# Kernel optimization log

Measured on AMD Instinct MI355X. Metric: run time of the kernel, lower is better.

The kernel has to match this reference:

```python
import jax, jax.numpy as jnp
import numpy as np

B, S, D_IN = 128, 196, 512
H, DK, RATIO = 8, 32, 4
DV = RATIO * DK                      # 128
QKV_DIM = H * (2 * DK + DV)          # 1536
PROJ_IN = H * DV                     # 1024
EPS = 1e-3                           # keras BatchNormalization default epsilon
SCALE = DK ** (-0.5)


def hard_swish(x):
    return x * jnp.clip(x + 3.0, 0.0, 6.0) * (1.0 / 6.0)


def setup_inputs() -> dict:
    key = jax.random.key(0)
    ks = jax.random.split(key, 12)
    inp = {
        "x": jax.random.normal(ks[0], (B, S, D_IN), dtype=jnp.float32),
        "W_qkv": jax.random.normal(ks[1], (D_IN, QKV_DIM), dtype=jnp.float32) * (D_IN ** -0.5),
        "b_qkv": jnp.zeros((QKV_DIM,), dtype=jnp.float32),
        "gamma1": jnp.ones((QKV_DIM,), dtype=jnp.float32),
        "beta1": jnp.zeros((QKV_DIM,), dtype=jnp.float32),
        "mean1": jax.random.normal(ks[2], (QKV_DIM,), dtype=jnp.float32) * 0.1,
        "var1": jax.random.uniform(ks[3], (QKV_DIM,), minval=0.5, maxval=1.5, dtype=jnp.float32),
        "W_proj": jax.random.normal(ks[4], (PROJ_IN, D_IN), dtype=jnp.float32) * (PROJ_IN ** -0.5),
        "b_proj": jnp.zeros((D_IN,), dtype=jnp.float32),
        "gamma2": jnp.ones((D_IN,), dtype=jnp.float32),
        "beta2": jnp.zeros((D_IN,), dtype=jnp.float32),
        "mean2": jax.random.normal(ks[5], (D_IN,), dtype=jnp.float32) * 0.1,
        "var2": jax.random.uniform(ks[6], (D_IN,), minval=0.5, maxval=1.5, dtype=jnp.float32),
    }
    return inp


def _bn(x, gamma, beta, mean, var):
    # inference-mode BatchNorm over the last (channel) axis
    return (x - mean) * jax.lax.rsqrt(var + EPS) * gamma + beta


def reference(x, W_qkv, b_qkv, gamma1, beta1, mean1, var1,
              W_proj, b_proj, gamma2, beta2, mean2, var2):
    # QKV projection + BN
    qkv = _bn(x @ W_qkv + b_qkv, gamma1, beta1, mean1, var1)      # [B,S,1536]
    qkv = qkv.reshape(B, S, H, 2 * DK + DV)
    q, k, v = jnp.split(qkv, [DK, 2 * DK], axis=3)                # [B,S,H,*]
    q = jnp.transpose(q, (0, 2, 1, 3))                            # [B,H,S,DK]
    k = jnp.transpose(k, (0, 2, 1, 3))
    v = jnp.transpose(v, (0, 2, 1, 3))                            # [B,H,S,DV]
    attn = jax.nn.softmax(jnp.einsum("bhqd,bhkd->bhqk", q, k) * SCALE, axis=-1)
    av = jnp.einsum("bhqk,bhkd->bhqd", attn, v)                   # [B,H,S,DV]
    # faithful to original: transpose to [B,H,DV,S] then reshape to [B,S,H*DV]
    hidden = jnp.transpose(av, (0, 1, 3, 2)).reshape(B, S, PROJ_IN)
    hidden = hard_swish(hidden)
    out = _bn(hidden @ W_proj + b_proj, gamma2, beta2, mean2, var2)  # [B,S,512]
    return out
```

## Files before the change

### kernel.cpp

```cpp
#include <hip/hip_runtime.h>
#include <math.h>

namespace {

constexpr int Bb   = 128;
constexpr int Ss   = 196;
constexpr int DIN  = 512;
constexpr int Hh   = 8;
constexpr int DKc  = 32;
constexpr int DVc  = 128;
constexpr int QKVD = 1536;
constexpr int PIN  = 1024;
constexpr int Mrows = Bb * Ss;
constexpr float EPSc   = 1e-3f;
constexpr float SCALEc = 0.17677669529663687f;

typedef __bf16 bf16x8 __attribute__((ext_vector_type(8)));
typedef __bf16 bf16x4 __attribute__((ext_vector_type(4)));
typedef float  f32x4  __attribute__((ext_vector_type(4)));

constexpr int VT_STRIDE = 232;
constexpr size_t VT_QELEMS = 8192;
constexpr size_t VT_BH = 4 * VT_QELEMS;

__device__ __forceinline__ void gl_lds16(const void* g, void* l) {
    __builtin_amdgcn_global_load_lds(
        (const __attribute__((address_space(1))) void*)g,
        (__attribute__((address_space(3))) void*)l, 16, 0, 0);
}

__global__ __launch_bounds__(256)
void cvt_f32_bf16(const float* __restrict__ in, __bf16* __restrict__ out, int n4)
{
    int i = blockIdx.x * 256 + threadIdx.x;
    if (i < n4) {
        float4 v = ((const float4*)in)[i];
        bf16x4 o = { (__bf16)v.x, (__bf16)v.y, (__bf16)v.z, (__bf16)v.w };
        ((bf16x4*)out)[i] = o;
    }
}

__global__ __launch_bounds__(256)
void transpose_cvt(const float* __restrict__ W, __bf16* __restrict__ WT, int K, int N)
{
    __shared__ float tile[32][33];
    const int n0 = blockIdx.x * 32, k0 = blockIdx.y * 32;
    const int tx = threadIdx.x & 31, ty = threadIdx.x >> 5;
#pragma unroll
    for (int i = ty; i < 32; i += 8)
        tile[i][tx] = W[(size_t)(k0 + i) * N + n0 + tx];
    __syncthreads();
#pragma unroll
    for (int i = ty; i < 32; i += 8)
        WT[(size_t)(n0 + i) * K + k0 + tx] = (__bf16)tile[tx][i];
}

__global__ __launch_bounds__(256)
void gemm1_bn_scatter(const __bf16* __restrict__ A, const __bf16* __restrict__ BT,
                      const float* __restrict__ bias, const float* __restrict__ gamma,
                      const float* __restrict__ beta, const float* __restrict__ mean,
                      const float* __restrict__ var,
                      __bf16* __restrict__ qkvO, __bf16* __restrict__ VTp)
{
    constexpr int N = QKVD, K = DIN;
    constexpr int BM = 128, BN = 128, BK = 32;
    __shared__ __bf16 As[BM * BK];
    __shared__ __bf16 Bs[BN * BK];

    const int t    = threadIdx.x;
    const int wave = t >> 6;
    const int lane = t & 63;
    const int lr   = lane & 15;
    const int q    = lane >> 4;

    constexpr int ntiles = N / BN;
    const int m0 = (int)(blockIdx.x / ntiles) * BM;
    const int n0 = (int)(blockIdx.x % ntiles) * BN;
    const int wm = (wave & 1) * 64;
    const int wn = (wave >> 1) * 64;

    const __bf16* aG0 = A  + (size_t)(m0 + (t >> 2)) * K + (t & 3) * 8;
    const __bf16* aG1 = aG0 + (size_t)64 * K;
    const __bf16* bG0 = BT + (size_t)(n0 + (t >> 2)) * K + (t & 3) * 8;
    const __bf16* bG1 = bG0 + (size_t)64 * K;
    char* lA = (char*)As + wave * 1024;
    char* lB = (char*)Bs + wave * 1024;

    f32x4 acc[4][4] = {};

    for (int k0 = 0; k0 < K; k0 += BK) {
        gl_lds16(aG0 + k0, lA);
        gl_lds16(aG1 + k0, lA + 4096);
        gl_lds16(bG0 + k0, lB);
        gl_lds16(bG1 + k0, lB + 4096);
        __syncthreads();
        bf16x8 aF[4], bF[4];
#pragma unroll
        for (int i = 0; i < 4; ++i)
            aF[i] = *(const bf16x8*)(As + (wm + i * 16 + lr) * 32 + q * 8);
#pragma unroll
        for (int j = 0; j < 4; ++j)
            bF[j] = *(const bf16x8*)(Bs + (wn + j * 16 + lr) * 32 + q * 8);
#pragma unroll
        for (int i = 0; i < 4; ++i)
#pragma unroll
            for (int j = 0; j < 4; ++j)
                acc[i][j] = __builtin_amdgcn_mfma_f32_16x16x32_bf16(
                    aF[i], bF[j], acc[i][j], 0, 0, 0);
        __syncthreads();
    }

    int bidx[4], sidx[4];
#pragma unroll
    for (int i = 0; i < 4; ++i) {
        int mrow = m0 + wm + i * 16 + q * 4;
        bidx[i] = mrow / 196;
        sidx[i] = mrow - bidx[i] * 196;
    }
#pragma unroll
    for (int j = 0; j < 4; ++j) {
        const int n  = n0 + wn + j * 16 + lr;
        const int h  = n / 192;
        const int ch = n - h * 192;
        const float s  = gamma[n] * rsqrtf(var[n] + EPSc);
        const float tv = fmaf(bias[n] - mean[n], s, beta[n]);
        if (ch < 64) {
#pragma unroll
            for (int i = 0; i < 4; ++i) {
                const int mrow = m0 + wm + i * 16 + q * 4;
#pragma unroll
                for (int r = 0; r < 4; ++r)
                    qkvO[(size_t)(mrow + r) * N + n] = (__bf16)fmaf(acc[i][j][r], s, tv);
            }
        } else {
            const int d = ch - 64;
#pragma unroll
            for (int i = 0; i < 4; ++i) {
                const size_t base = (size_t)(bidx[i] * 8 + h) * VT_BH
                                  + (size_t)(d >> 5) * VT_QELEMS
                                  + (size_t)(d & 31) * VT_STRIDE + sidx[i];
                bf16x4 pk = { (__bf16)fmaf(acc[i][j][0], s, tv),
                              (__bf16)fmaf(acc[i][j][1], s, tv),
                              (__bf16)fmaf(acc[i][j][2], s, tv),
                              (__bf16)fmaf(acc[i][j][3], s, tv) };
                *(bf16x4*)(VTp + base) = pk;
            }
        }
    }
}

template<int N, int K>
__global__ __launch_bounds__(256)
void gemm_bn_mfma(const __bf16* __restrict__ A, const __bf16* __restrict__ BT,
                  const float* __restrict__ bias, const float* __restrict__ gamma,
                  const float* __restrict__ beta, const float* __restrict__ mean,
                  const float* __restrict__ var, float* __restrict__ C)
{
    constexpr int BM = 128, BN = 128, BK = 32;
    __shared__ __bf16 As[BM * BK];
    __shared__ __bf16 Bs[BN * BK];
    const int t    = threadIdx.x;
    const int wave = t >> 6;
    const int lane = t & 63;
    const int lr   = lane & 15;
    const int q    = lane >> 4;
    constexpr int ntiles = N / BN;
    const int m0 = (int)(blockIdx.x / ntiles) * BM;
    const int n0 = (int)(blockIdx.x % ntiles) * BN;
    const int wm = (wave & 1) * 64;
    const int wn = (wave >> 1) * 64;
    const __bf16* aG0 = A  + (size_t)(m0 + (t >> 2)) * K + (t & 3) * 8;
    const __bf16* aG1 = aG0 + (size_t)64 * K;
    const __bf16* bG0 = BT + (size_t)(n0 + (t >> 2)) * K + (t & 3) * 8;
    const __bf16* bG1 = bG0 + (size_t)64 * K;
    char* lA = (char*)As + wave * 1024;
    char* lB = (char*)Bs + wave * 1024;
    f32x4 acc[4][4] = {};
    for (int k0 = 0; k0 < K; k0 += BK) {
        gl_lds16(aG0 + k0, lA);
        gl_lds16(aG1 + k0, lA + 4096);
        gl_lds16(bG0 + k0, lB);
        gl_lds16(bG1 + k0, lB + 4096);
        __syncthreads();
        bf16x8 aF[4], bF[4];
#pragma unroll
        for (int i = 0; i < 4; ++i)
            aF[i] = *(const bf16x8*)(As + (wm + i * 16 + lr) * 32 + q * 8);
#pragma unroll
        for (int j = 0; j < 4; ++j)
            bF[j] = *(const bf16x8*)(Bs + (wn + j * 16 + lr) * 32 + q * 8);
#pragma unroll
        for (int i = 0; i < 4; ++i)
#pragma unroll
            for (int j = 0; j < 4; ++j)
                acc[i][j] = __builtin_amdgcn_mfma_f32_16x16x32_bf16(
                    aF[i], bF[j], acc[i][j], 0, 0, 0);
        __syncthreads();
    }
#pragma unroll
    for (int j = 0; j < 4; ++j) {
        const int n = n0 + wn + j * 16 + lr;
        const float s  = gamma[n] * rsqrtf(var[n] + EPSc);
        const float tv = fmaf(bias[n] - mean[n], s, beta[n]);
#pragma unroll
        for (int i = 0; i < 4; ++i) {
            const int mrow = m0 + wm + i * 16 + q * 4;
#pragma unroll
            for (int r = 0; r < 4; ++r)
                C[(size_t)(mrow + r) * N + n] = fmaf(acc[i][j][r], s, tv);
        }
    }
}

__global__ __launch_bounds__(1024)
void attn_mfma(const __bf16* __restrict__ qkv, const __bf16* __restrict__ VTp,
               __bf16* __restrict__ hidden)
{
    __shared__ __align__(16) char smem[145920];
    __bf16* Kb = (__bf16*)smem;

    const int t = threadIdx.x;
    const int wave = t >> 6, lane = t & 63;
    const int lr = lane & 15, q = lane >> 4;
    const int bh = blockIdx.x;
    const int b = bh >> 3, h = bh & 7;
    const __bf16* qkvb = qkv + (size_t)b * 196 * QKVD + h * 192;

    const char* gV = (const char*)(VTp + (size_t)bh * VT_BH);
    char* ldsV = smem + 113152;
    gl_lds16(gV + wave * 1024 + lane * 16, ldsV + wave * 1024);

    if (t < 196 * 4) {
        const int s = t >> 2, c = t & 3;
        bf16x8 v = *(const bf16x8*)(qkvb + (size_t)s * QKVD + 32 + c * 8);
        *(bf16x8*)(Kb + s * 40 + c * 8) = v;
    }

    __syncthreads();

    const int qt = wave;
    const bool wactive = (qt <= 12);
    __bf16* Pw = (__bf16*)(smem + 16640 + (wactive ? qt : 0) * 7424);

    if (wactive) {
        int sQ = qt * 16 + lr; if (sQ > 195) sQ = 195;
        bf16x8 aQ = *(const bf16x8*)(qkv + ((size_t)b * 196 + sQ) * QKVD + h * 192 + q * 8);

        f32x4 sc[13];
#pragma unroll
        for (int nt = 0; nt < 13; ++nt) {
            bf16x8 bK = *(const bf16x8*)(Kb + (nt * 16 + lr) * 40 + q * 8);
            f32x4 z = {0.f, 0.f, 0.f, 0.f};
            sc[nt] = __builtin_amdgcn_mfma_f32_16x16x32_bf16(aQ, bK, z, 0, 0, 0);
        }
        float mrow[4] = {-1e30f, -1e30f, -1e30f, -1e30f};
#pragma unroll
        for (int nt = 0; nt < 13; ++nt) {
            const bool valid = (nt < 12) | (lr < 4);
#pragma unroll
            for (int r = 0; r < 4; ++r) {
                float x = sc[nt][r] * SCALEc;
                sc[nt][r] = x;
                if (valid) mrow[r] = fmaxf(mrow[r], x);
            }
        }
#pragma unroll
        for (int d = 1; d < 16; d <<= 1)
#pragma unroll
            for (int r = 0; r < 4; ++r)
                mrow[r] = fmaxf(mrow[r], __shfl_xor(mrow[r], d, 64));
        float l[4] = {0.f, 0.f, 0.f, 0.f};
#pragma unroll
        for (int nt = 0; nt < 13; ++nt) {
            const bool valid = (nt < 12) | (lr < 4);
#pragma unroll
            for (int r = 0; r < 4; ++r) {
                float e = valid ? __expf(sc[nt][r] - mrow[r]) : 0.f;
                sc[nt][r] = e;
                l[r] += e;
            }
        }
#pragma unroll
        for (int d = 1; d < 16; d <<= 1)
#pragma unroll
            for (int r = 0; r < 4; ++r)
                l[r] += __shfl_xor(l[r], d, 64);
        float inv[4];
#pragma unroll
        for (int r = 0; r < 4; ++r) inv[r] = 1.f / l[r];

#pragma unroll
        for (int nt = 0; nt < 13; ++nt)
#pragma unroll
            for (int r = 0; r < 4; ++r)
                Pw[(q * 4 + r) * 232 + nt * 16 + lr] = (__bf16)(sc[nt][r] * inv[r]);
        for (int idx = lane; idx < 16 * 24; idx += 64) {
            int row = idx & 15, cz = 208 + (idx >> 4);
            Pw[row * 232 + cz] = (__bf16)0.f;
        }
    }
    __syncthreads();

    const int sbase = qt * 16 + q * 4;
    const bool sval = wactive && (sbase + 3 < 196);
    __bf16* hb = hidden + (size_t)b * 200704 + (size_t)h * 25088;

    for (int q4 = 0; q4 < 4; ++q4) {
        const __bf16* Vl = (const __bf16*)(ldsV + (q4 & 1) * 16384);
        if (q4 < 3)
            gl_lds16(gV + (size_t)(q4 + 1) * 16384 + wave * 1024 + lane * 16,
                     ldsV + ((q4 + 1) & 1) * 16384 + wave * 1024);
        if (wactive) {
            f32x4 o0 = {0.f, 0.f, 0.f, 0.f}, o1 = {0.f, 0.f, 0.f, 0.f};
#pragma unroll
            for (int kk = 0; kk < 7; ++kk) {
                bf16x8 aP = *(const bf16x8*)(Pw + lr * 232 + kk * 32 + q * 8);
                bf16x8 b0 = *(const bf16x8*)(Vl + lr * 232 + kk * 32 + q * 8);
                bf16x8 b1 = *(const bf16x8*)(Vl + (16 + lr) * 232 + kk * 32 + q * 8);
                o0 = __builtin_amdgcn_mfma_f32_16x16x32_bf16(aP, b0, o0, 0, 0, 0);
                o1 = __builtin_amdgcn_mfma_f32_16x16x32_bf16(aP, b1, o1, 0, 0, 0);
            }
            if (sval) {
#pragma unroll
                for (int nt2 = 0; nt2 < 2; ++nt2) {
                    f32x4 o = nt2 ? o1 : o0;
                    const int d = q4 * 32 + nt2 * 16 + lr;
                    bf16x4 pk;
#pragma unroll
                    for (int r = 0; r < 4; ++r) {
                        float x = o[r];
                        pk[r] = (__bf16)(x * fminf(fmaxf(x + 3.f, 0.f), 6.f) * (1.f / 6.f));
                    }
                    *(bf16x4*)(hb + (size_t)d * 196 + sbase) = pk;
                }
            }
        }
        if (q4 < 3) __syncthreads();
    }
}

}

extern "C" void kernel_launch(void* const* d_in, const int* in_sizes, int n_in,
                              void* d_out, int out_size, void* d_ws, size_t ws_size,
                              hipStream_t stream)
{
    const float* x    = (const float*)d_in[0];
    const float* Wqkv = (const float*)d_in[1];
    const float* bqkv = (const float*)d_in[2];
    const float* g1   = (const float*)d_in[3];
    const float* be1  = (const float*)d_in[4];
    const float* mu1  = (const float*)d_in[5];
    const float* va1  = (const float*)d_in[6];
    const float* Wp   = (const float*)d_in[7];
    const float* bp   = (const float*)d_in[8];
    const float* g2   = (const float*)d_in[9];
    const float* be2  = (const float*)d_in[10];
    const float* mu2  = (const float*)d_in[11];
    const float* va2  = (const float*)d_in[12];

    char* ws = (char*)d_ws;
    __bf16* qkv    = (__bf16*)ws;
    __bf16* VTp    = (__bf16*)(ws + 77070336);
    __bf16* hidden = (__bf16*)(ws + 144179200);
    __bf16* xb     = (__bf16*)(ws + 195559424);
    __bf16* WT1    = (__bf16*)(ws + 221249536);
    __bf16* WT2    = (__bf16*)(ws + 222822400);
    float*  out    = (float*)d_out;

    cvt_f32_bf16<<<dim3((Mrows * DIN / 4 + 255) / 256), dim3(256), 0, stream>>>(
        x, xb, Mrows * DIN / 4);
    transpose_cvt<<<dim3(QKVD / 32, DIN / 32), dim3(256), 0, stream>>>(Wqkv, WT1, DIN, QKVD);
    transpose_cvt<<<dim3(DIN / 32, PIN / 32), dim3(256), 0, stream>>>(Wp, WT2, PIN, DIN);

    gemm1_bn_scatter<<<dim3(196 * (QKVD / 128)), dim3(256), 0, stream>>>(
        xb, WT1, bqkv, g1, be1, mu1, va1, qkv, VTp);

    attn_mfma<<<dim3(Bb * Hh), dim3(1024), 0, stream>>>(qkv, VTp, hidden);

    gemm_bn_mfma<DIN, PIN><<<dim3(196 * (DIN / 128)), dim3(256), 0, stream>>>(
        hidden, WT2, bp, g2, be2, mu2, va2, out);
}
```

Measured before the change: 307.1 us.

## Widen GEMM K-step to 64, remap blocks across XCDs, use nontemporal stores

Both GEMM kernels now load a 64-wide K slice per barrier pair in two LDS halves, which halves the number of __syncthreads per tile. Block IDs are permuted so consecutive tiles are spread across the 8 XCDs, aiming for better L2 locality. Output stores in the GEMMs and the attention kernel use nontemporal hints. The changes double LDS use per block and hard-code 196 M-tiles in the remap, which only suits grids of that size.

```diff
diff --git a/kernel.cpp b/kernel.cpp
--- a/kernel.cpp
+++ b/kernel.cpp
@@ -63,9 +63,9 @@
                       __bf16* __restrict__ qkvO, __bf16* __restrict__ VTp)
 {
     constexpr int N = QKVD, K = DIN;
-    constexpr int BM = 128, BN = 128, BK = 32;
-    __shared__ __bf16 As[BM * BK];
-    __shared__ __bf16 Bs[BN * BK];
+    constexpr int BM = 128, BN = 128;
+    __shared__ __bf16 As[2][BM * 32];
+    __shared__ __bf16 Bs[2][BN * 32];
 
     const int t    = threadIdx.x;
     const int wave = t >> 6;
@@ -74,8 +74,10 @@
     const int q    = lane >> 4;
 
     constexpr int ntiles = N / BN;
-    const int m0 = (int)(blockIdx.x / ntiles) * BM;
-    const int n0 = (int)(blockIdx.x % ntiles) * BN;
+    constexpr int nwg = 196 * ntiles;
+    const int bid = (blockIdx.x & 7) * (nwg >> 3) + (blockIdx.x >> 3);
+    const int m0 = (bid / ntiles) * BM;
+    const int n0 = (bid % ntiles) * BN;
     const int wm = (wave & 1) * 64;
     const int wn = (wave >> 1) * 64;
 
@@ -88,25 +90,32 @@
 
     f32x4 acc[4][4] = {};
 
-    for (int k0 = 0; k0 < K; k0 += BK) {
-        gl_lds16(aG0 + k0, lA);
-        gl_lds16(aG1 + k0, lA + 4096);
-        gl_lds16(bG0 + k0, lB);
-        gl_lds16(bG1 + k0, lB + 4096);
+    for (int k0 = 0; k0 < K; k0 += 64) {
+        gl_lds16(aG0 + k0,      lA);
+        gl_lds16(aG1 + k0,      lA + 4096);
+        gl_lds16(aG0 + k0 + 32, lA + 8192);
+        gl_lds16(aG1 + k0 + 32, lA + 8192 + 4096);
+        gl_lds16(bG0 + k0,      lB);
+        gl_lds16(bG1 + k0,      lB + 4096);
+        gl_lds16(bG0 + k0 + 32, lB + 8192);
+        gl_lds16(bG1 + k0 + 32, lB + 8192 + 4096);
         __syncthreads();
-        bf16x8 aF[4], bF[4];
-#pragma unroll
-        for (int i = 0; i < 4; ++i)
-            aF[i] = *(const bf16x8*)(As + (wm + i * 16 + lr) * 32 + q * 8);
-#pragma unroll
-        for (int j = 0; j < 4; ++j)
-            bF[j] = *(const bf16x8*)(Bs + (wn + j * 16 + lr) * 32 + q * 8);
-#pragma unroll
-        for (int i = 0; i < 4; ++i)
+#pragma unroll
+        for (int kk = 0; kk < 2; ++kk) {
+            bf16x8 aF[4], bF[4];
+#pragma unroll
+            for (int i = 0; i < 4; ++i)
+                aF[i] = *(const bf16x8*)(&As[kk][(wm + i * 16 + lr) * 32 + q * 8]);
 #pragma unroll
             for (int j = 0; j < 4; ++j)
-                acc[i][j] = __builtin_amdgcn_mfma_f32_16x16x32_bf16(
-                    aF[i], bF[j], acc[i][j], 0, 0, 0);
+                bF[j] = *(const bf16x8*)(&Bs[kk][(wn + j * 16 + lr) * 32 + q * 8]);
+#pragma unroll
+            for (int i = 0; i < 4; ++i)
+#pragma unroll
+                for (int j = 0; j < 4; ++j)
+                    acc[i][j] = __builtin_amdgcn_mfma_f32_16x16x32_bf16(
+                        aF[i], bF[j], acc[i][j], 0, 0, 0);
+        }
         __syncthreads();
     }
 
@@ -130,7 +139,9 @@
                 const int mrow = m0 + wm + i * 16 + q * 4;
 #pragma unroll
                 for (int r = 0; r < 4; ++r)
-                    qkvO[(size_t)(mrow + r) * N + n] = (__bf16)fmaf(acc[i][j][r], s, tv);
+                    __builtin_nontemporal_store(
+                        (__bf16)fmaf(acc[i][j][r], s, tv),
+                        &qkvO[(size_t)(mrow + r) * N + n]);
             }
         } else {
             const int d = ch - 64;
@@ -143,7 +154,7 @@
                               (__bf16)fmaf(acc[i][j][1], s, tv),
                               (__bf16)fmaf(acc[i][j][2], s, tv),
                               (__bf16)fmaf(acc[i][j][3], s, tv) };
-                *(bf16x4*)(VTp + base) = pk;
+                __builtin_nontemporal_store(pk, (bf16x4*)(VTp + base));
             }
         }
     }
@@ -156,17 +167,19 @@
                   const float* __restrict__ beta, const float* __restrict__ mean,
                   const float* __restrict__ var, float* __restrict__ C)
 {
-    constexpr int BM = 128, BN = 128, BK = 32;
-    __shared__ __bf16 As[BM * BK];
-    __shared__ __bf16 Bs[BN * BK];
+    constexpr int BM = 128, BN = 128;
+    __shared__ __bf16 As[2][BM * 32];
+    __shared__ __bf16 Bs[2][BN * 32];
     const int t    = threadIdx.x;
     const int wave = t >> 6;
     const int lane = t & 63;
     const int lr   = lane & 15;
     const int q    = lane >> 4;
     constexpr int ntiles = N / BN;
-    const int m0 = (int)(blockIdx.x / ntiles) * BM;
-    const int n0 = (int)(blockIdx.x % ntiles) * BN;
+    constexpr int nwg = 196 * ntiles;
+    const int bid = (blockIdx.x & 7) * (nwg >> 3) + (blockIdx.x >> 3);
+    const int m0 = (bid / ntiles) * BM;
+    const int n0 = (bid % ntiles) * BN;
     const int wm = (wave & 1) * 64;
     const int wn = (wave >> 1) * 64;
     const __bf16* aG0 = A  + (size_t)(m0 + (t >> 2)) * K + (t & 3) * 8;
@@ -176,25 +189,32 @@
     char* lA = (char*)As + wave * 1024;
     char* lB = (char*)Bs + wave * 1024;
     f32x4 acc[4][4] = {};
-    for (int k0 = 0; k0 < K; k0 += BK) {
-        gl_lds16(aG0 + k0, lA);
-        gl_lds16(aG1 + k0, lA + 4096);
-        gl_lds16(bG0 + k0, lB);
-        gl_lds16(bG1 + k0, lB + 4096);
+    for (int k0 = 0; k0 < K; k0 += 64) {
+        gl_lds16(aG0 + k0,      lA);
+        gl_lds16(aG1 + k0,      lA + 4096);
+        gl_lds16(aG0 + k0 + 32, lA + 8192);
+        gl_lds16(aG1 + k0 + 32, lA + 8192 + 4096);
+        gl_lds16(bG0 + k0,      lB);
+        gl_lds16(bG1 + k0,      lB + 4096);
+        gl_lds16(bG0 + k0 + 32, lB + 8192);
+        gl_lds16(bG1 + k0 + 32, lB + 8192 + 4096);
         __syncthreads();
-        bf16x8 aF[4], bF[4];
-#pragma unroll
-        for (int i = 0; i < 4; ++i)
-            aF[i] = *(const bf16x8*)(As + (wm + i * 16 + lr) * 32 + q * 8);
-#pragma unroll
-        for (int j = 0; j < 4; ++j)
-            bF[j] = *(const bf16x8*)(Bs + (wn + j * 16 + lr) * 32 + q * 8);
-#pragma unroll
-        for (int i = 0; i < 4; ++i)
+#pragma unroll
+        for (int kk = 0; kk < 2; ++kk) {
+            bf16x8 aF[4], bF[4];
+#pragma unroll
+            for (int i = 0; i < 4; ++i)
+                aF[i] = *(const bf16x8*)(&As[kk][(wm + i * 16 + lr) * 32 + q * 8]);
 #pragma unroll
             for (int j = 0; j < 4; ++j)
-                acc[i][j] = __builtin_amdgcn_mfma_f32_16x16x32_bf16(
-                    aF[i], bF[j], acc[i][j], 0, 0, 0);
+                bF[j] = *(const bf16x8*)(&Bs[kk][(wn + j * 16 + lr) * 32 + q * 8]);
+#pragma unroll
+            for (int i = 0; i < 4; ++i)
+#pragma unroll
+                for (int j = 0; j < 4; ++j)
+                    acc[i][j] = __builtin_amdgcn_mfma_f32_16x16x32_bf16(
+                        aF[i], bF[j], acc[i][j], 0, 0, 0);
+        }
         __syncthreads();
     }
 #pragma unroll
@@ -207,7 +227,9 @@
             const int mrow = m0 + wm + i * 16 + q * 4;
 #pragma unroll
             for (int r = 0; r < 4; ++r)
-                C[(size_t)(mrow + r) * N + n] = fmaf(acc[i][j][r], s, tv);
+                __builtin_nontemporal_store(
+                    fmaf(acc[i][j][r], s, tv),
+                    &C[(size_t)(mrow + r) * N + n]);
         }
     }
 }
@@ -331,7 +353,7 @@
                         float x = o[r];
                         pk[r] = (__bf16)(x * fminf(fmaxf(x + 3.f, 0.f), 6.f) * (1.f / 6.f));
                     }
-                    *(bf16x4*)(hb + (size_t)d * 196 + sbase) = pk;
+                    __builtin_nontemporal_store(pk, (bf16x4*)(hb + (size_t)d * 196 + sbase));
                 }
             }
         }
```

Result: slower. 350.6 us (+14.2%).
